# Kernel optimization log

Measured on AMD Instinct MI355X. Metric: run time of the kernel, lower is better.

## Reference

```python
import jax, jax.numpy as jnp
import numpy as np

HEADS = 16
LN_EPS = 1e-5


def setup_inputs() -> dict:
    key = jax.random.key(0)
    ks = jax.random.split(key, 12)
    B, IMG, Q, H = 8192, 2048, 768, 1024
    def init(k, shape, fan_in):
        return jax.random.normal(k, shape, dtype=jnp.float32) * (fan_in ** -0.5)
    return {
        "features1": jax.random.normal(ks[0], (B, IMG), dtype=jnp.float32),
        "features2": jax.random.normal(ks[1], (B, Q), dtype=jnp.float32),
        "W1": init(ks[2], (IMG, H), IMG),
        "b1": jnp.zeros((H,), dtype=jnp.float32),
        "W2": init(ks[3], (Q, H), Q),
        "b2": jnp.zeros((H,), dtype=jnp.float32),
        "Wqkv": init(ks[4], (H, 3 * H), H),
        "Wout": init(ks[5], (H, H), H),
        "bout": jnp.zeros((H,), dtype=jnp.float32),
        "gamma": jnp.ones((2 * H,), dtype=jnp.float32),
        "beta": jnp.zeros((2 * H,), dtype=jnp.float32),
    }


def reference(features1, features2, W1, b1, W2, b2, Wqkv, Wout, bout, gamma, beta):
    B = features1.shape[0]
    H = W1.shape[1]
    hd = H // HEADS
    scale = hd ** -0.5
    # modality projections -> [B, H] each
    f1 = features1 @ W1 + b1
    f2 = features2 @ W2 + b2
    x = jnp.stack([f1, f2], axis=1)                      # [B, 2, H]
    qkv = x @ Wqkv                                       # [B, 2, 3H]
    q, k, v = jnp.split(qkv, 3, axis=-1)
    # b n (h d) -> b h n d
    def to_heads(t):
        return t.reshape(B, 2, HEADS, hd).transpose(0, 2, 1, 3)
    q, k, v = to_heads(q) * scale, to_heads(k), to_heads(v)
    attn = jnp.einsum('bhid,bhjd->bhij', q, k)           # [B, h, 2, 2]
    attn = jax.nn.softmax(attn, axis=-1)
    out = jnp.einsum('bhij,bhjd->bhid', attn, v)         # [B, h, 2, d]
    out = out.transpose(0, 2, 1, 3).reshape(B, 2, H)     # b h n d -> b n (h d)
    out = out @ Wout + bout                              # [B, 2, H]
    flat = out.reshape(B, 2 * H)
    # LayerNorm over last dim
    mu = jnp.mean(flat, axis=-1, keepdims=True)
    var = jnp.var(flat, axis=-1, keepdims=True)
    normed = (flat - mu) * jax.lax.rsqrt(var + LN_EPS) * gamma + beta
    # dropout in eval mode = identity
    res = jnp.concatenate([f1, f2], axis=1)              # [B, 2H]
    return normed + res
```

## Files before the change

### kernel.cpp

```cpp
#include <hip/hip_runtime.h>
#include <hip/hip_bf16.h>
#include <cstdint>

typedef __attribute__((ext_vector_type(8))) short short8;
typedef __attribute__((ext_vector_type(4))) short short4v;
typedef __attribute__((ext_vector_type(4))) float floatx4;
typedef __attribute__((ext_vector_type(4))) unsigned short ushort4v;

__device__ __forceinline__ float bf2f(unsigned short u) {
    union { unsigned int u; float f; } v;
    v.u = ((unsigned int)u) << 16;
    return v.f;
}
__device__ __forceinline__ unsigned short f2bf(float f) {
    union { float f; unsigned int u; } v; v.f = f;
    unsigned int u = v.u;
    unsigned int r = (u + 0x7FFFu + ((u >> 16) & 1u)) >> 16;
    return (unsigned short)r;
}
__device__ __forceinline__ float lo_bf(unsigned int u) {
    union { unsigned int u; float f; } v; v.u = u << 16; return v.f;
}
__device__ __forceinline__ float hi_bf(unsigned int u) {
    union { unsigned int u; float f; } v; v.u = u & 0xffff0000u; return v.f;
}
__device__ __forceinline__ void gld_lds16(const void* g, void* l) {
    __builtin_amdgcn_global_load_lds(
        (const __attribute__((address_space(1))) unsigned int*)g,
        (__attribute__((address_space(3))) unsigned int*)l,
        16, 0, 0);
}

__global__ __launch_bounds__(256) void prep_kernel(
    const float* __restrict__ f1, const float* __restrict__ f2,
    unsigned short* __restrict__ f1b, unsigned short* __restrict__ f2b,
    const float* __restrict__ W1, unsigned short* __restrict__ W1t,
    const float* __restrict__ W2, unsigned short* __restrict__ W2t,
    const float* __restrict__ Wqkv, unsigned short* __restrict__ Wqkvt,
    const float* __restrict__ Wout, unsigned short* __restrict__ Woutt) {
    __shared__ float tile[64][33];
    const int b = blockIdx.x;
    const int tid = threadIdx.x;

    if (b < 5632) {
        const float* in = (b < 4096) ? f1 : f2;
        unsigned short* outp = (b < 4096) ? f1b : f2b;
        int base = ((b < 4096) ? b : (b - 4096)) * 1024 + tid;
#pragma unroll
        for (int it = 0; it < 4; it++) {
            int i = base + it * 256;
            float4 v = ((const float4*)in)[i];
            ushort4v o;
            o.x = f2bf(v.x); o.y = f2bf(v.y); o.z = f2bf(v.z); o.w = f2bf(v.w);
            ((ushort4v*)outp)[i] = o;
        }
        return;
    }

    const float* in; unsigned short* outp; int K, N, t;
    if (b < 6656)      { in = W1;   outp = W1t;   K = 2048; N = 1024; t = b - 5632; }
    else if (b < 7040) { in = W2;   outp = W2t;   K = 768;  N = 1024; t = b - 6656; }
    else if (b < 8576) { in = Wqkv; outp = Wqkvt; K = 1024; N = 3072; t = b - 7040; }
    else               { in = Wout; outp = Woutt; K = 1024; N = 1024; t = b - 8576; }
    const int ntiles = N >> 5;
    const int n0 = (t % ntiles) * 32;
    const int k0 = (t / ntiles) * 64;
    const int tx = tid & 31, tg = tid >> 5;
#pragma unroll
    for (int i = 0; i < 8; i++)
        tile[tg * 8 + i][tx] = in[(size_t)(k0 + tg * 8 + i) * N + n0 + tx];
    __syncthreads();
    const int n = tid >> 3, kc = (tid & 7) * 8;
    short8 o;
#pragma unroll
    for (int j = 0; j < 8; j++) o[j] = (short)f2bf(tile[kc + j][n]);
    *(short8*)&outp[(size_t)(n0 + n) * K + k0 + kc] = o;
}

template <bool OUT_BF16, bool HAS_BIAS>
__device__ __forceinline__ void gemm_core(const unsigned short* __restrict__ A,
                                          const unsigned short* __restrict__ Bt,
                                          void* __restrict__ Cv, const float* __restrict__ bias,
                                          int K, int ldc, int blockM, int blockN,
                                          unsigned short* As, unsigned short* Bs) {
    const int tid  = threadIdx.x;
    const int lane = tid & 63;
    const int wave = tid >> 6;
    const int wm = wave >> 1, wn = wave & 1;

    const unsigned short* gA = A  + (size_t)(blockM + (tid >> 2)) * K + (tid & 3) * 8;
    const unsigned short* gB = Bt + (size_t)(blockN + (tid >> 2)) * K + (tid & 3) * 8;
    const size_t sK = (size_t)64 * K;
    unsigned short* lA = As + wave * 512;
    unsigned short* lB = Bs + wave * 512;

    floatx4 acc[4][4];
#pragma unroll
    for (int i = 0; i < 4; i++)
#pragma unroll
        for (int j = 0; j < 4; j++) acc[i][j] = (floatx4){0.f, 0.f, 0.f, 0.f};

    const int col  = lane & 15;
    const int quad = lane >> 4;
    const int aoff32 = (wm * 64 + col) * 32 + quad * 8;
    const int boff32 = (wn * 64 + col) * 32 + quad * 8;

    const int kIters = K >> 6;
    for (int kt = 0; kt < kIters; ++kt) {
        const size_t ko = (size_t)kt * 64;
        gld_lds16(gA + ko,           lA);
        gld_lds16(gA + sK + ko,      lA + 2048);
        gld_lds16(gA + 32 + ko,      lA + 4096);
        gld_lds16(gA + sK + 32 + ko, lA + 6144);
        gld_lds16(gB + ko,           lB);
        gld_lds16(gB + sK + ko,      lB + 2048);
        gld_lds16(gB + 32 + ko,      lB + 4096);
        gld_lds16(gB + sK + 32 + ko, lB + 6144);
        __syncthreads();

#pragma unroll
        for (int hh = 0; hh < 2; hh++) {
            short8 a[4];
#pragma unroll
            for (int i = 0; i < 4; i++) a[i] = *(const short8*)&As[hh * 4096 + aoff32 + i * 512];
#pragma unroll
            for (int j = 0; j < 4; j++) {
                short8 bj = *(const short8*)&Bs[hh * 4096 + boff32 + j * 512];
#pragma unroll
                for (int i = 0; i < 4; i++)
                    acc[i][j] = __builtin_amdgcn_mfma_f32_16x16x32_bf16(a[i], bj, acc[i][j], 0, 0, 0);
            }
        }
        __syncthreads();
    }

#pragma unroll
    for (int i = 0; i < 4; i++) {
#pragma unroll
        for (int j = 0; j < 4; j++) {
#pragma unroll
            for (int r = 0; r < 4; r++) {
                int row = blockM + wm * 64 + i * 16 + quad * 4 + r;
                int cn  = blockN + wn * 64 + j * 16 + col;
                float v = acc[i][j][r];
                if (HAS_BIAS) v += bias[cn];
                if (OUT_BF16) ((unsigned short*)Cv)[(size_t)row * ldc + cn] = f2bf(v);
                else          ((float*)Cv)[(size_t)row * ldc + cn] = v;
            }
        }
    }
}

__global__ __launch_bounds__(256, 3)
void gemm_f12(const unsigned short* __restrict__ f1b, const unsigned short* __restrict__ W1t,
              const float* __restrict__ b1,
              const unsigned short* __restrict__ f2b, const unsigned short* __restrict__ W2t,
              const float* __restrict__ b2, unsigned short* __restrict__ xb) {
    __shared__ alignas(16) unsigned short As[8192];
    __shared__ alignas(16) unsigned short Bs[8192];
    const int blockM = blockIdx.x * 128;
    const int blockN = blockIdx.y * 128;
    if (blockIdx.z == 0)
        gemm_core<true, true>(f1b, W1t, (void*)xb, b1, 2048, 2048, blockM, blockN, As, Bs);
    else
        gemm_core<true, true>(f2b, W2t, (void*)(xb + 1024), b2, 768, 2048, blockM, blockN, As, Bs);
}

__global__ __launch_bounds__(256, 3)
void gemm_proj(const unsigned short* __restrict__ attn, const unsigned short* __restrict__ Woutt,
               const float* __restrict__ bout, unsigned short* __restrict__ projb) {
    __shared__ alignas(16) unsigned short As[8192];
    __shared__ alignas(16) unsigned short Bs[8192];
    gemm_core<true, true>(attn, Woutt, (void*)projb, bout, 1024, 1024,
                          blockIdx.x * 128, blockIdx.y * 128, As, Bs);
}

#define T2_STRIDE 132
__global__ __launch_bounds__(256, 3)
void gemm_qkv_attn(const unsigned short* __restrict__ A, const unsigned short* __restrict__ Bt,
                   unsigned short* __restrict__ attn_out) {
    __shared__ alignas(16) char smem[52224];
    unsigned short* As = (unsigned short*)smem;
    unsigned short* Bs = As + 8192;
    unsigned short* T2 = (unsigned short*)smem;
    float* wsm = (float*)(smem + 50688);

    const int tid  = threadIdx.x;
    const int lane = tid & 63;
    const int wave = tid >> 6;
    const int g = blockIdx.x;
    const int h = g >> 7;
    const int blockM = (g & 127) * 128;
    const int wm = wave >> 1, wn = wave & 1;
    const int K = 1024;

    const unsigned short* gA = A  + (size_t)(blockM + (tid >> 2)) * K + (tid & 3) * 8;
    const unsigned short* gB = Bt + (size_t)(h * 64 + (tid >> 2)) * K + (tid & 3) * 8;
    unsigned short* lA = As + wave * 512;
    unsigned short* lB = Bs + wave * 512;

    floatx4 acc[4][6];
#pragma unroll
    for (int i = 0; i < 4; i++)
#pragma unroll
        for (int j = 0; j < 6; j++) acc[i][j] = (floatx4){0.f, 0.f, 0.f, 0.f};

    const int col  = lane & 15;
    const int quad = lane >> 4;
    const int aoff32 = (wm * 64 + col) * 32 + quad * 8;
    const int boff32 = (wn * 96 + col) * 32 + quad * 8;

    for (int kt = 0; kt < 16; ++kt) {
        const size_t ko = (size_t)kt * 64;
        gld_lds16(gA + ko,               lA);
        gld_lds16(gA + 65536 + ko,       lA + 2048);
        gld_lds16(gA + 32 + ko,          lA + 4096);
        gld_lds16(gA + 65536 + 32 + ko,  lA + 6144);
        gld_lds16(gB + ko,               lB);
        gld_lds16(gB + 1048576 + ko,     lB + 2048);
        gld_lds16(gB + 2097152 + ko,     lB + 4096);
        gld_lds16(gB + 32 + ko,          lB + 6144);
        gld_lds16(gB + 1048576 + 32 + ko, lB + 8192);
        gld_lds16(gB + 2097152 + 32 + ko, lB + 10240);
        __syncthreads();

#pragma unroll
        for (int hh = 0; hh < 2; hh++) {
            short8 a[4];
#pragma unroll
            for (int i = 0; i < 4; i++) a[i] = *(const short8*)&As[hh * 4096 + aoff32 + i * 512];
#pragma unroll
            for (int j = 0; j < 6; j++) {
                short8 bj = *(const short8*)&Bs[hh * 6144 + boff32 + j * 512];
#pragma unroll
                for (int i = 0; i < 4; i++)
                    acc[i][j] = __builtin_amdgcn_mfma_f32_16x16x32_bf16(a[i], bj, acc[i][j], 0, 0, 0);
            }
        }
        __syncthreads();
    }

#pragma unroll
    for (int i = 0; i < 4; i++) {
#pragma unroll
        for (int j = 0; j < 6; j++) {
            int c  = wn * 96 + j * 16 + col;
            int r0 = wm * 64 + i * 16 + quad * 4;
            short4v pk;
            pk.x = (short)f2bf(acc[i][j][0]);
            pk.y = (short)f2bf(acc[i][j][1]);
            pk.z = (short)f2bf(acc[i][j][2]);
            pk.w = (short)f2bf(acc[i][j][3]);
            *(short4v*)&T2[c * T2_STRIDE + r0] = pk;
        }
    }
    __syncthreads();

    if (tid < 64) {
        const int ib = tid;
        float s00 = 0.f, s01 = 0.f, s10 = 0.f, s11 = 0.f;
#pragma unroll 8
        for (int d = 0; d < 64; d++) {
            unsigned int qp = *(const unsigned int*)&T2[d * T2_STRIDE + 2 * ib];
            unsigned int kp = *(const unsigned int*)&T2[(64 + d) * T2_STRIDE + 2 * ib];
            float q0 = lo_bf(qp), q1 = hi_bf(qp);
            float k0 = lo_bf(kp), k1 = hi_bf(kp);
            s00 += q0 * k0; s01 += q0 * k1;
            s10 += q1 * k0; s11 += q1 * k1;
        }
        const float sc = 0.125f;
        s00 *= sc; s01 *= sc; s10 *= sc; s11 *= sc;
        float m0 = fmaxf(s00, s01), m1 = fmaxf(s10, s11);
        float e00 = __expf(s00 - m0), e01 = __expf(s01 - m0);
        float e10 = __expf(s10 - m1), e11 = __expf(s11 - m1);
        float i0 = 1.f / (e00 + e01), i1 = 1.f / (e10 + e11);
        wsm[ib * 4 + 0] = e00 * i0; wsm[ib * 4 + 1] = e01 * i0;
        wsm[ib * 4 + 2] = e10 * i1; wsm[ib * 4 + 3] = e11 * i1;
    }
    __syncthreads();

#pragma unroll
    for (int gg = 0; gg < 4; gg++) {
        int chunk = gg * 256 + tid;
        int r = chunk >> 3;
        int dc = (chunk & 7) * 8;
        int ib = r >> 1, n = r & 1;
        float w0 = wsm[ib * 4 + n * 2 + 0];
        float w1 = wsm[ib * 4 + n * 2 + 1];
        short8 o;
#pragma unroll
        for (int dd = 0; dd < 8; dd++) {
            unsigned int vp = *(const unsigned int*)&T2[(128 + dc + dd) * T2_STRIDE + 2 * ib];
            o[dd] = (short)f2bf(w0 * lo_bf(vp) + w1 * hi_bf(vp));
        }
        *(short8*)&attn_out[(size_t)(blockM + r) * 1024 + h * 64 + dc] = o;
    }
}

__global__ __launch_bounds__(256) void ln_res_kernel(const unsigned short* __restrict__ proj,
                                                     const unsigned short* __restrict__ xres,
                                                     const float* __restrict__ gamma,
                                                     const float* __restrict__ beta,
                                                     float* __restrict__ out) {
    const int b = blockIdx.x;
    const int tid = threadIdx.x;
    const size_t base = (size_t)b * 2048;
    short8 p8 = ((const short8*)(proj + base))[tid];
    float pv[8];
#pragma unroll
    for (int e = 0; e < 8; e++) pv[e] = bf2f((unsigned short)p8[e]);
    float s = 0.f, ss = 0.f;
#pragma unroll
    for (int e = 0; e < 8; e++) { s += pv[e]; ss += pv[e] * pv[e]; }
#pragma unroll
    for (int off = 32; off > 0; off >>= 1) {
        s  += __shfl_xor(s, off);
        ss += __shfl_xor(ss, off);
    }
    __shared__ float red[8];
    const int wave = tid >> 6;
    if ((tid & 63) == 0) { red[wave] = s; red[4 + wave] = ss; }
    __syncthreads();
    s  = red[0] + red[1] + red[2] + red[3];
    ss = red[4] + red[5] + red[6] + red[7];
    const float mean = s * (1.0f / 2048.0f);
    const float var  = ss * (1.0f / 2048.0f) - mean * mean;
    const float rstd = rsqrtf(var + 1e-5f);

    const float4* g4 = (const float4*)gamma;
    const float4* b4 = (const float4*)beta;
    float4 g0 = g4[2 * tid], g1 = g4[2 * tid + 1];
    float4 be0 = b4[2 * tid], be1 = b4[2 * tid + 1];
    short8 r8 = ((const short8*)(xres + base))[tid];
    float4 o0, o1;
    o0.x = (pv[0] - mean) * rstd * g0.x + be0.x + bf2f((unsigned short)r8[0]);
    o0.y = (pv[1] - mean) * rstd * g0.y + be0.y + bf2f((unsigned short)r8[1]);
    o0.z = (pv[2] - mean) * rstd * g0.z + be0.z + bf2f((unsigned short)r8[2]);
    o0.w = (pv[3] - mean) * rstd * g0.w + be0.w + bf2f((unsigned short)r8[3]);
    o1.x = (pv[4] - mean) * rstd * g1.x + be1.x + bf2f((unsigned short)r8[4]);
    o1.y = (pv[5] - mean) * rstd * g1.y + be1.y + bf2f((unsigned short)r8[5]);
    o1.z = (pv[6] - mean) * rstd * g1.z + be1.z + bf2f((unsigned short)r8[6]);
    o1.w = (pv[7] - mean) * rstd * g1.w + be1.w + bf2f((unsigned short)r8[7]);
    float4* op = (float4*)(out + base);
    op[2 * tid] = o0;
    op[2 * tid + 1] = o1;
}

extern "C" void kernel_launch(void* const* d_in, const int* in_sizes, int n_in,
                              void* d_out, int out_size, void* d_ws, size_t ws_size,
                              hipStream_t stream) {
    (void)in_sizes; (void)n_in; (void)out_size; (void)ws_size;
    const float* features1 = (const float*)d_in[0];
    const float* features2 = (const float*)d_in[1];
    const float* W1   = (const float*)d_in[2];
    const float* b1   = (const float*)d_in[3];
    const float* W2   = (const float*)d_in[4];
    const float* b2   = (const float*)d_in[5];
    const float* Wqkv = (const float*)d_in[6];
    const float* Wout = (const float*)d_in[7];
    const float* bout = (const float*)d_in[8];
    const float* gamma = (const float*)d_in[9];
    const float* beta  = (const float*)d_in[10];
    float* out = (float*)d_out;

    char* ws = (char*)d_ws;
    unsigned short* f1b   = (unsigned short*)(ws);
    unsigned short* f2b   = (unsigned short*)(ws + 33554432);
    unsigned short* W1t   = (unsigned short*)(ws + 46137344);
    unsigned short* W2t   = (unsigned short*)(ws + 50331648);
    unsigned short* Wqkvt = (unsigned short*)(ws + 51904512);
    unsigned short* Woutt = (unsigned short*)(ws + 58195968);
    unsigned short* xb    = (unsigned short*)(ws + 60293120);
    unsigned short* attn  = (unsigned short*)(ws + 93847552);
    unsigned short* projb = (unsigned short*)(ws + 127401984);

    prep_kernel<<<9088, 256, 0, stream>>>(features1, features2, f1b, f2b,
                                          W1, W1t, W2, W2t, Wqkv, Wqkvt, Wout, Woutt);
    gemm_f12<<<dim3(64, 8, 2), 256, 0, stream>>>(f1b, W1t, b1, f2b, W2t, b2, xb);
    gemm_qkv_attn<<<2048, 256, 0, stream>>>(xb, Wqkvt, attn);
    gemm_proj<<<dim3(128, 8), 256, 0, stream>>>(attn, Woutt, bout, projb);
    ln_res_kernel<<<8192, 256, 0, stream>>>(projb, xb, gamma, beta, out);
}
```

Before: 376.9 us.

## Switch GEMMs to 32x32x16 MFMA with XOR-swizzled row-major LDS tiles

All three GEMM paths (modality projections, QKV+attention, output projection) now use the 32x32x16 bf16 MFMA instead of 16x16x32. The LDS tile layout changes from a split-K 32-wide layout to full 64-wide rows, with an XOR swizzle on the 8-element chunk index to avoid bank conflicts. The larger MFMA needs fewer LDS fragment reads per FLOP and fewer instructions. The epilogue and T2 staging are adapted to the 32x32 accumulator layout, which makes the output stores less contiguous per lane.

New measurement: 394.4 us. 4.6% more time.

```diff
diff --git a/kernel.cpp b/kernel.cpp
--- a/kernel.cpp
+++ b/kernel.cpp
@@ -5,6 +5,7 @@
 typedef __attribute__((ext_vector_type(8))) short short8;
 typedef __attribute__((ext_vector_type(4))) short short4v;
 typedef __attribute__((ext_vector_type(4))) float floatx4;
+typedef __attribute__((ext_vector_type(16))) float floatx16;
 typedef __attribute__((ext_vector_type(4))) unsigned short ushort4v;
 
 __device__ __forceinline__ float bf2f(unsigned short u) {
@@ -78,70 +79,77 @@
 }
 
 template <bool OUT_BF16, bool HAS_BIAS>
-__device__ __forceinline__ void gemm_core(const unsigned short* __restrict__ A,
-                                          const unsigned short* __restrict__ Bt,
-                                          void* __restrict__ Cv, const float* __restrict__ bias,
-                                          int K, int ldc, int blockM, int blockN,
-                                          unsigned short* As, unsigned short* Bs) {
+__device__ __forceinline__ void gemm_core32(const unsigned short* __restrict__ A,
+                                            const unsigned short* __restrict__ Bt,
+                                            void* __restrict__ Cv, const float* __restrict__ bias,
+                                            int K, int ldc, int blockM, int blockN,
+                                            unsigned short* As, unsigned short* Bs) {
     const int tid  = threadIdx.x;
     const int lane = tid & 63;
     const int wave = tid >> 6;
     const int wm = wave >> 1, wn = wave & 1;
 
-    const unsigned short* gA = A  + (size_t)(blockM + (tid >> 2)) * K + (tid & 3) * 8;
-    const unsigned short* gB = Bt + (size_t)(blockN + (tid >> 2)) * K + (tid & 3) * 8;
-    const size_t sK = (size_t)64 * K;
+    const int srow = tid >> 3;
+    const int sch  = ((tid & 7) ^ (srow & 7)) * 8;
+    const unsigned short* gA = A  + (size_t)(blockM + srow) * K + sch;
+    const unsigned short* gB = Bt + (size_t)(blockN + srow) * K + sch;
+    const size_t rK = (size_t)32 * K;
     unsigned short* lA = As + wave * 512;
     unsigned short* lB = Bs + wave * 512;
 
-    floatx4 acc[4][4];
-#pragma unroll
-    for (int i = 0; i < 4; i++)
-#pragma unroll
-        for (int j = 0; j < 4; j++) acc[i][j] = (floatx4){0.f, 0.f, 0.f, 0.f};
-
-    const int col  = lane & 15;
-    const int quad = lane >> 4;
-    const int aoff32 = (wm * 64 + col) * 32 + quad * 8;
-    const int boff32 = (wn * 64 + col) * 32 + quad * 8;
+    floatx16 acc[2][2];
+#pragma unroll
+    for (int i = 0; i < 2; i++)
+#pragma unroll
+        for (int j = 0; j < 2; j++)
+#pragma unroll
+            for (int r = 0; r < 16; r++) acc[i][j][r] = 0.f;
+
+    const int r31 = lane & 31;
+    const int hi  = lane >> 5;
+    int sx[4];
+#pragma unroll
+    for (int s = 0; s < 4; s++) sx[s] = ((s * 2 + hi) ^ (lane & 7)) * 8;
 
     const int kIters = K >> 6;
     for (int kt = 0; kt < kIters; ++kt) {
         const size_t ko = (size_t)kt * 64;
-        gld_lds16(gA + ko,           lA);
-        gld_lds16(gA + sK + ko,      lA + 2048);
-        gld_lds16(gA + 32 + ko,      lA + 4096);
-        gld_lds16(gA + sK + 32 + ko, lA + 6144);
-        gld_lds16(gB + ko,           lB);
-        gld_lds16(gB + sK + ko,      lB + 2048);
-        gld_lds16(gB + 32 + ko,      lB + 4096);
-        gld_lds16(gB + sK + 32 + ko, lB + 6144);
+        gld_lds16(gA + ko,            lA);
+        gld_lds16(gA + rK + ko,       lA + 2048);
+        gld_lds16(gA + 2 * rK + ko,   lA + 4096);
+        gld_lds16(gA + 3 * rK + ko,   lA + 6144);
+        gld_lds16(gB + ko,            lB);
+        gld_lds16(gB + rK + ko,       lB + 2048);
+        gld_lds16(gB + 2 * rK + ko,   lB + 4096);
+        gld_lds16(gB + 3 * rK + ko,   lB + 6144);
         __syncthreads();
 
 #pragma unroll
-        for (int hh = 0; hh < 2; hh++) {
-            short8 a[4];
-#pragma unroll
-            for (int i = 0; i < 4; i++) a[i] = *(const short8*)&As[hh * 4096 + aoff32 + i * 512];
-#pragma unroll
-            for (int j = 0; j < 4; j++) {
-                short8 bj = *(const short8*)&Bs[hh * 4096 + boff32 + j * 512];
-#pragma unroll
-                for (int i = 0; i < 4; i++)
-                    acc[i][j] = __builtin_amdgcn_mfma_f32_16x16x32_bf16(a[i], bj, acc[i][j], 0, 0, 0);
-            }
+        for (int s = 0; s < 4; s++) {
+            short8 af[2], bf[2];
+#pragma unroll
+            for (int i = 0; i < 2; i++)
+                af[i] = *(const short8*)&As[(wm * 64 + i * 32 + r31) * 64 + sx[s]];
+#pragma unroll
+            for (int j = 0; j < 2; j++)
+                bf[j] = *(const short8*)&Bs[(wn * 64 + j * 32 + r31) * 64 + sx[s]];
+#pragma unroll
+            for (int j = 0; j < 2; j++)
+#pragma unroll
+                for (int i = 0; i < 2; i++)
+                    acc[i][j] = __builtin_amdgcn_mfma_f32_32x32x16_bf16(af[i], bf[j], acc[i][j], 0, 0, 0);
         }
         __syncthreads();
     }
 
 #pragma unroll
-    for (int i = 0; i < 4; i++) {
-#pragma unroll
-        for (int j = 0; j < 4; j++) {
-#pragma unroll
-            for (int r = 0; r < 4; r++) {
-                int row = blockM + wm * 64 + i * 16 + quad * 4 + r;
-                int cn  = blockN + wn * 64 + j * 16 + col;
+    for (int i = 0; i < 2; i++) {
+#pragma unroll
+        for (int j = 0; j < 2; j++) {
+            const int cn = blockN + wn * 64 + j * 32 + r31;
+#pragma unroll
+            for (int r = 0; r < 16; r++) {
+                int row = blockM + wm * 64 + i * 32 + (r & 3) + 8 * (r >> 2) + 4 * hi;
                 float v = acc[i][j][r];
                 if (HAS_BIAS) v += bias[cn];
                 if (OUT_BF16) ((unsigned short*)Cv)[(size_t)row * ldc + cn] = f2bf(v);
@@ -161,9 +169,9 @@
     const int blockM = blockIdx.x * 128;
     const int blockN = blockIdx.y * 128;
     if (blockIdx.z == 0)
-        gemm_core<true, true>(f1b, W1t, (void*)xb, b1, 2048, 2048, blockM, blockN, As, Bs);
+        gemm_core32<true, true>(f1b, W1t, (void*)xb, b1, 2048, 2048, blockM, blockN, As, Bs);
     else
-        gemm_core<true, true>(f2b, W2t, (void*)(xb + 1024), b2, 768, 2048, blockM, blockN, As, Bs);
+        gemm_core32<true, true>(f2b, W2t, (void*)(xb + 1024), b2, 768, 2048, blockM, blockN, As, Bs);
 }
 
 __global__ __launch_bounds__(256, 3)
@@ -171,19 +179,19 @@
                const float* __restrict__ bout, unsigned short* __restrict__ projb) {
     __shared__ alignas(16) unsigned short As[8192];
     __shared__ alignas(16) unsigned short Bs[8192];
-    gemm_core<true, true>(attn, Woutt, (void*)projb, bout, 1024, 1024,
-                          blockIdx.x * 128, blockIdx.y * 128, As, Bs);
-}
-
-#define T2_STRIDE 132
+    gemm_core32<true, true>(attn, Woutt, (void*)projb, bout, 1024, 1024,
+                            blockIdx.x * 128, blockIdx.y * 128, As, Bs);
+}
+
+#define T2_ST 132
 __global__ __launch_bounds__(256, 3)
-void gemm_qkv_attn(const unsigned short* __restrict__ A, const unsigned short* __restrict__ Bt,
-                   unsigned short* __restrict__ attn_out) {
+void gemm_qkv_attn4(const unsigned short* __restrict__ A, const unsigned short* __restrict__ Bt,
+                    unsigned short* __restrict__ attn_out) {
     __shared__ alignas(16) char smem[52224];
     unsigned short* As = (unsigned short*)smem;
     unsigned short* Bs = As + 8192;
     unsigned short* T2 = (unsigned short*)smem;
-    float* wsm = (float*)(smem + 50688);
+    float* wsm = (float*)(smem + 51200);
 
     const int tid  = threadIdx.x;
     const int lane = tid & 63;
@@ -194,64 +202,75 @@
     const int wm = wave >> 1, wn = wave & 1;
     const int K = 1024;
 
-    const unsigned short* gA = A  + (size_t)(blockM + (tid >> 2)) * K + (tid & 3) * 8;
-    const unsigned short* gB = Bt + (size_t)(h * 64 + (tid >> 2)) * K + (tid & 3) * 8;
+    const int srow = tid >> 3;
+    const int sch  = ((tid & 7) ^ (srow & 7)) * 8;
+    const unsigned short* gA = A  + (size_t)(blockM + srow) * K + sch;
+    const unsigned short* gB = Bt + (size_t)(h * 64 + srow) * K + sch;
+    const size_t rK = (size_t)32 * K;
     unsigned short* lA = As + wave * 512;
     unsigned short* lB = Bs + wave * 512;
 
-    floatx4 acc[4][6];
-#pragma unroll
-    for (int i = 0; i < 4; i++)
-#pragma unroll
-        for (int j = 0; j < 6; j++) acc[i][j] = (floatx4){0.f, 0.f, 0.f, 0.f};
-
-    const int col  = lane & 15;
-    const int quad = lane >> 4;
-    const int aoff32 = (wm * 64 + col) * 32 + quad * 8;
-    const int boff32 = (wn * 96 + col) * 32 + quad * 8;
+    floatx16 acc[2][3];
+#pragma unroll
+    for (int i = 0; i < 2; i++)
+#pragma unroll
+        for (int j = 0; j < 3; j++)
+#pragma unroll
+            for (int r = 0; r < 16; r++) acc[i][j][r] = 0.f;
+
+    const int r31 = lane & 31;
+    const int hi  = lane >> 5;
+    int sx[4];
+#pragma unroll
+    for (int s = 0; s < 4; s++) sx[s] = ((s * 2 + hi) ^ (lane & 7)) * 8;
 
     for (int kt = 0; kt < 16; ++kt) {
         const size_t ko = (size_t)kt * 64;
-        gld_lds16(gA + ko,               lA);
-        gld_lds16(gA + 65536 + ko,       lA + 2048);
-        gld_lds16(gA + 32 + ko,          lA + 4096);
-        gld_lds16(gA + 65536 + 32 + ko,  lA + 6144);
-        gld_lds16(gB + ko,               lB);
-        gld_lds16(gB + 1048576 + ko,     lB + 2048);
-        gld_lds16(gB + 2097152 + ko,     lB + 4096);
-        gld_lds16(gB + 32 + ko,          lB + 6144);
-        gld_lds16(gB + 1048576 + 32 + ko, lB + 8192);
-        gld_lds16(gB + 2097152 + 32 + ko, lB + 10240);
+        gld_lds16(gA + ko,                  lA);
+        gld_lds16(gA + rK + ko,             lA + 2048);
+        gld_lds16(gA + 2 * rK + ko,         lA + 4096);
+        gld_lds16(gA + 3 * rK + ko,         lA + 6144);
+        gld_lds16(gB + ko,                  lB);
+        gld_lds16(gB + rK + ko,             lB + 2048);
+        gld_lds16(gB + 1048576 + ko,        lB + 4096);
+        gld_lds16(gB + 1048576 + rK + ko,   lB + 6144);
+        gld_lds16(gB + 2097152 + ko,        lB + 8192);
+        gld_lds16(gB + 2097152 + rK + ko,   lB + 10240);
         __syncthreads();
 
 #pragma unroll
-        for (int hh = 0; hh < 2; hh++) {
-            short8 a[4];
-#pragma unroll
-            for (int i = 0; i < 4; i++) a[i] = *(const short8*)&As[hh * 4096 + aoff32 + i * 512];
-#pragma unroll
-            for (int j = 0; j < 6; j++) {
-                short8 bj = *(const short8*)&Bs[hh * 6144 + boff32 + j * 512];
-#pragma unroll
-                for (int i = 0; i < 4; i++)
-                    acc[i][j] = __builtin_amdgcn_mfma_f32_16x16x32_bf16(a[i], bj, acc[i][j], 0, 0, 0);
+        for (int s = 0; s < 4; s++) {
+            short8 af[2], bf[3];
+#pragma unroll
+            for (int i = 0; i < 2; i++)
+                af[i] = *(const short8*)&As[(wm * 64 + i * 32 + r31) * 64 + sx[s]];
+#pragma unroll
+            for (int j = 0; j < 3; j++)
+                bf[j] = *(const short8*)&Bs[(wn * 96 + j * 32 + r31) * 64 + sx[s]];
+#pragma unroll
+            for (int j = 0; j < 3; j++)
+#pragma unroll
+                for (int i = 0; i < 2; i++)
+                    acc[i][j] = __builtin_amdgcn_mfma_f32_32x32x16_bf16(af[i], bf[j], acc[i][j], 0, 0, 0);
+        }
+        __syncthreads();
+    }
+
+#pragma unroll
+    for (int i = 0; i < 2; i++) {
+#pragma unroll
+        for (int j = 0; j < 3; j++) {
+            const int c = wn * 96 + j * 32 + r31;
+#pragma unroll
+            for (int g2 = 0; g2 < 4; g2++) {
+                int r0 = wm * 64 + i * 32 + g2 * 8 + 4 * hi;
+                short4v pk;
+                pk.x = (short)f2bf(acc[i][j][g2 * 4 + 0]);
+                pk.y = (short)f2bf(acc[i][j][g2 * 4 + 1]);
+                pk.z = (short)f2bf(acc[i][j][g2 * 4 + 2]);
+                pk.w = (short)f2bf(acc[i][j][g2 * 4 + 3]);
+                *(short4v*)&T2[c * T2_ST + r0] = pk;
             }
-        }
-        __syncthreads();
-    }
-
-#pragma unroll
-    for (int i = 0; i < 4; i++) {
-#pragma unroll
-        for (int j = 0; j < 6; j++) {
-            int c  = wn * 96 + j * 16 + col;
-            int r0 = wm * 64 + i * 16 + quad * 4;
-            short4v pk;
-            pk.x = (short)f2bf(acc[i][j][0]);
-            pk.y = (short)f2bf(acc[i][j][1]);
-            pk.z = (short)f2bf(acc[i][j][2]);
-            pk.w = (short)f2bf(acc[i][j][3]);
-            *(short4v*)&T2[c * T2_STRIDE + r0] = pk;
         }
     }
     __syncthreads();
@@ -261,8 +280,8 @@
         float s00 = 0.f, s01 = 0.f, s10 = 0.f, s11 = 0.f;
 #pragma unroll 8
         for (int d = 0; d < 64; d++) {
-            unsigned int qp = *(const unsigned int*)&T2[d * T2_STRIDE + 2 * ib];
-            unsigned int kp = *(const unsigned int*)&T2[(64 + d) * T2_STRIDE + 2 * ib];
+            unsigned int qp = *(const unsigned int*)&T2[d * T2_ST + 2 * ib];
+            unsigned int kp = *(const unsigned int*)&T2[(64 + d) * T2_ST + 2 * ib];
             float q0 = lo_bf(qp), q1 = hi_bf(qp);
             float k0 = lo_bf(kp), k1 = hi_bf(kp);
             s00 += q0 * k0; s01 += q0 * k1;
@@ -290,7 +309,7 @@
         short8 o;
 #pragma unroll
         for (int dd = 0; dd < 8; dd++) {
-            unsigned int vp = *(const unsigned int*)&T2[(128 + dc + dd) * T2_STRIDE + 2 * ib];
+            unsigned int vp = *(const unsigned int*)&T2[(128 + dc + dd) * T2_ST + 2 * ib];
             o[dd] = (short)f2bf(w0 * lo_bf(vp) + w1 * hi_bf(vp));
         }
         *(short8*)&attn_out[(size_t)(blockM + r) * 1024 + h * 64 + dc] = o;
@@ -377,7 +396,7 @@
     prep_kernel<<<9088, 256, 0, stream>>>(features1, features2, f1b, f2b,
                                           W1, W1t, W2, W2t, Wqkv, Wqkvt, Wout, Woutt);
     gemm_f12<<<dim3(64, 8, 2), 256, 0, stream>>>(f1b, W1t, b1, f2b, W2t, b2, xb);
-    gemm_qkv_attn<<<2048, 256, 0, stream>>>(xb, Wqkvt, attn);
+    gemm_qkv_attn4<<<2048, 256, 0, stream>>>(xb, Wqkvt, attn);
     gemm_proj<<<dim3(128, 8), 256, 0, stream>>>(attn, Woutt, bout, projb);
     ln_res_kernel<<<8192, 256, 0, stream>>>(projb, xb, gamma, beta, out);
 }
```
